# Performance work log

Hardware: AMD Instinct MI355X
Metric: run time of the kernel (lower is better)

## Reference

```python
import jax, jax.numpy as jnp
import numpy as np

DIM = 512
HEADS = 8
DH = DIM // HEADS          # 64
SCALE = DH ** (-0.5)
B, H, W = 8, 64, 64        # N = 4096, H and W multiples of 8 -> exact adaptive pool
N = H * W
POOL = 8                   # AdaptiveAvgPool2d((8,8)) -> 64 pooled tokens


def setup_inputs() -> dict:
    key = jax.random.key(0)
    ks = jax.random.split(key, 6)
    return {
        "x": jax.random.normal(ks[0], (B, N, DIM), dtype=jnp.float32),
        "proj_w": jax.random.normal(ks[1], (DIM, DIM), dtype=jnp.float32) * (DIM ** -0.5),
        "step_rep": jax.random.normal(ks[2], (HEADS, 1, 1), dtype=jnp.float32),
        "step_x": jax.random.normal(ks[3], (HEADS, 1, 1), dtype=jnp.float32),
        "to_out_w": jax.random.normal(ks[4], (DIM, DIM), dtype=jnp.float32) * (DIM ** -0.5),
        "to_out_b": jax.random.normal(ks[5], (DIM,), dtype=jnp.float32),
    }


def reference(x, proj_w, step_rep, step_x, to_out_w, to_out_b):
    b, n, c = x.shape
    # proj (Linear, no bias): w = x @ proj_w.T
    w = jnp.einsum('bnc,dc->bnd', x, proj_w)                       # [B,N,C]
    # AdaptiveAvgPool2d to (8,8): exact block mean since H,W % 8 == 0
    bh, bw = H // POOL, W // POOL
    rep = w.reshape(b, POOL, bh, POOL, bw, c).mean(axis=(2, 4))    # [B,8,8,C]
    rep = rep.reshape(b, POOL * POOL, c)                           # [B,64,C]
    # split heads: [B,h,tokens,dh]
    wh = w.reshape(b, n, HEADS, DH).transpose(0, 2, 1, 3)          # [B,h,N,dh]
    reph = rep.reshape(b, POOL * POOL, HEADS, DH).transpose(0, 2, 1, 3)  # [B,h,64,dh]
    # cross-attention: pooled queries vs full tokens (attn is reused later)
    dots = jnp.einsum('bhqd,bhkd->bhqk', reph, wh) * SCALE         # [B,h,64,N]
    attn = jax.nn.softmax(dots, axis=-1)
    rep_delta = jnp.einsum('bhqk,bhkd->bhqd', attn, wh)            # [B,h,64,dh]
    reph = reph + step_rep * rep_delta
    # self-attention among pooled reps
    dots2 = jnp.einsum('bhqd,bhkd->bhqk', reph, reph) * SCALE      # [B,h,64,64]
    attn2 = jax.nn.softmax(dots2, axis=-1)
    x_delta = jnp.einsum('bhqk,bhkd->bhqd', attn2, reph)           # [B,h,64,dh]
    # upsample back to tokens by reusing attn transposed
    x_delta = jnp.einsum('bhqn,bhqd->bhnd', attn, x_delta)         # [B,h,N,dh]
    x_delta = step_x * x_delta
    x_delta = x_delta.transpose(0, 2, 1, 3).reshape(b, n, c)       # [B,N,C]
    out = jnp.einsum('bnc,dc->bnd', x_delta, to_out_w) + to_out_b
    return out
```

## Files before the change

### kernel.cpp

```cpp
#include <hip/hip_runtime.h>
#include <hip/hip_bf16.h>
#include <stdint.h>

typedef __attribute__((ext_vector_type(8))) short short8v;
typedef __attribute__((ext_vector_type(4))) float floatx4;
typedef __attribute__((ext_vector_type(4))) unsigned uintx4;

#define DEV __device__ __forceinline__

DEV ushort f2bf(float f) {
  union { float f; unsigned u; } v; v.f = f;
  unsigned r = v.u + 0x7fffu + ((v.u >> 16) & 1u);
  return (ushort)(r >> 16);
}
DEV float bf2f(ushort b) {
  union { unsigned u; float f; } v; v.u = ((unsigned)b) << 16;
  return v.f;
}
DEV unsigned cvtpk(float lo, float hi) {
  unsigned r;
  asm("v_cvt_pk_bf16_f32 %0, %1, %2" : "=v"(r) : "v"(lo), "v"(hi));
  return r;
}
DEV int swz(int row, int colByte) {
  return row * 128 + (colByte ^ ((row & 7) << 4));
}
DEV int swz256(int row, int colByte) {
  return row * 256 + (colByte ^ ((row & 7) << 4));
}
DEV floatx4 mfma16(short8v a, short8v b, floatx4 c) {
  return __builtin_amdgcn_mfma_f32_16x16x32_bf16(a, b, c, 0, 0, 0);
}

#define GLD_LDS16(g, l)                                                   \
  __builtin_amdgcn_global_load_lds(                                       \
      (const __attribute__((address_space(1))) void*)(g),                 \
      (__attribute__((address_space(3))) void*)(l), 16, 0, 0)

#define WAIT_LGKM0 asm volatile("s_waitcnt lgkmcnt(0)" ::: "memory")
DEV void sbar() {
  __builtin_amdgcn_sched_barrier(0);
  __builtin_amdgcn_s_barrier();
  __builtin_amdgcn_sched_barrier(0);
}

constexpr int Bc = 8, HEADS = 8, NTOK = 4096, CDIM = 512, DH = 64;
constexpr float SCALE = 0.125f;
constexpr int NCH = 8, CHK = 512;

__global__ __launch_bounds__(512, 2) void k_gemm1(const float* __restrict__ A,
                                                  const float* __restrict__ Bw,
                                                  ushort* __restrict__ Cout) {
  __shared__ ushort sA[2][256 * 64];
  __shared__ ushort sB[2][256 * 64];
  const int t = threadIdx.x;
  const int w = t >> 6, l = t & 63;
  const int lg = l >> 4, li = l & 15;
  const int bid = blockIdx.x;
  const int f = (bid & 7) * 32 + (bid >> 3);
  const int m0 = (f >> 1) * 256, n0 = (f & 1) * 256;
  const int wr = (w >> 2) * 128, wc = (w & 3) * 64;

  float4 fa[8];
  float4 fb[8];

  auto loadA = [&](int kt) {
#pragma unroll
    for (int i = 0; i < 4; ++i) {
      int s = i * 512 + t, row = s >> 3, pch = s & 7;
      const float* g = A + (size_t)(m0 + row) * CDIM + kt * 64 + pch * 8;
      fa[2 * i] = *(const float4*)g;
      fa[2 * i + 1] = *(const float4*)(g + 4);
    }
  };
  auto loadB = [&](int kt) {
#pragma unroll
    for (int i = 0; i < 4; ++i) {
      int s = i * 512 + t, row = s >> 3, pch = s & 7;
      const float* g = Bw + (size_t)(n0 + row) * CDIM + kt * 64 + pch * 8;
      fb[2 * i] = *(const float4*)g;
      fb[2 * i + 1] = *(const float4*)(g + 4);
    }
  };
  auto writeAB = [&](int buf) {
#pragma unroll
    for (int i = 0; i < 4; ++i) {
      int s = i * 512 + t, row = s >> 3, pch = s & 7;
      int off = row * 128 + ((pch ^ (row & 7)) << 4);
      uintx4 pk;
      pk.x = cvtpk(fa[2 * i].x, fa[2 * i].y);
      pk.y = cvtpk(fa[2 * i].z, fa[2 * i].w);
      pk.z = cvtpk(fa[2 * i + 1].x, fa[2 * i + 1].y);
      pk.w = cvtpk(fa[2 * i + 1].z, fa[2 * i + 1].w);
      *(uintx4*)((char*)sA[buf] + off) = pk;
      uintx4 qk;
      qk.x = cvtpk(fb[2 * i].x, fb[2 * i].y);
      qk.y = cvtpk(fb[2 * i].z, fb[2 * i].w);
      qk.z = cvtpk(fb[2 * i + 1].x, fb[2 * i + 1].y);
      qk.w = cvtpk(fb[2 * i + 1].z, fb[2 * i + 1].w);
      *(uintx4*)((char*)sB[buf] + off) = qk;
    }
  };

  floatx4 acc[8][4] = {};

  loadA(0); loadB(0);
  writeAB(0);
  loadA(1); loadB(1);
  WAIT_LGKM0;
  sbar();

#pragma unroll
  for (int kt = 0; kt < 8; ++kt) {
    const int cur = kt & 1;
    if (kt < 7) writeAB(cur ^ 1);
    if (kt < 6) { loadA(kt + 2); loadB(kt + 2); }
#pragma unroll
    for (int kk = 0; kk < 2; ++kk) {
      int colb = (kk * 32 + lg * 8) * 2;
      short8v bf[4];
#pragma unroll
      for (int n = 0; n < 4; ++n)
        bf[n] = *(const short8v*)((const char*)sB[cur] + swz(wc + n * 16 + li, colb));
#pragma unroll
      for (int mh = 0; mh < 2; ++mh) {
        short8v af[4];
#pragma unroll
        for (int m = 0; m < 4; ++m)
          af[m] = *(const short8v*)((const char*)sA[cur] + swz(wr + mh * 64 + m * 16 + li, colb));
#pragma unroll
        for (int m = 0; m < 4; ++m)
#pragma unroll
          for (int n = 0; n < 4; ++n)
            acc[mh * 4 + m][n] = mfma16(af[m], bf[n], acc[mh * 4 + m][n]);
      }
    }
    if (kt < 7) { WAIT_LGKM0; sbar(); }
  }

#pragma unroll
  for (int m = 0; m < 8; ++m)
#pragma unroll
    for (int n = 0; n < 4; ++n) {
      int col = n0 + wc + n * 16 + li;
#pragma unroll
      for (int r = 0; r < 4; ++r) {
        int row = m0 + wr + m * 16 + lg * 4 + r;
        Cout[(size_t)row * CDIM + col] = f2bf(acc[m][n][r]);
      }
    }
}

__global__ __launch_bounds__(512, 2) void k_gemm3(const ushort* __restrict__ attnT,
                                                  const ushort* __restrict__ M2T,
                                                  float* __restrict__ out,
                                                  const float* __restrict__ bias) {
  __shared__ ushort sA[2][256 * 64];
  __shared__ ushort sB[2][256 * 64];
  const int t = threadIdx.x;
  const int w = t >> 6, l = t & 63;
  const int lg = l >> 4, li = l & 15;
  const int bid = blockIdx.x;
  const int b = bid & 7;
  const int idx = bid >> 3;
  const int m0 = (idx >> 1) * 256, n0 = (idx & 1) * 256;
  const int wr = (w >> 2) * 128, wc = (w & 3) * 64;
  const ushort* Bb = M2T + (size_t)b * 262144;

  short8v fA[4], fB[4];
  auto loadAB = [&](int kt) {
#pragma unroll
    for (int i = 0; i < 4; ++i) {
      int s = i * 512 + t, row = s >> 3, pch = s & 7;
      fA[i] = *(const short8v*)(attnT + (((size_t)(b * 8 + kt)) * NTOK + m0 + row) * 64 + pch * 8);
      fB[i] = *(const short8v*)(Bb + (size_t)(n0 + row) * CDIM + kt * 64 + pch * 8);
    }
  };
  auto writeAB = [&](int buf) {
#pragma unroll
    for (int i = 0; i < 4; ++i) {
      int s = i * 512 + t, row = s >> 3, pch = s & 7;
      int off = row * 128 + ((pch ^ (row & 7)) << 4);
      *(short8v*)((char*)sA[buf] + off) = fA[i];
      *(short8v*)((char*)sB[buf] + off) = fB[i];
    }
  };

  floatx4 acc[8][4] = {};

  loadAB(0);
  writeAB(0);
  loadAB(1);
  WAIT_LGKM0;
  sbar();

#pragma unroll
  for (int kt = 0; kt < 8; ++kt) {
    const int cur = kt & 1;
    if (kt < 7) writeAB(cur ^ 1);
    if (kt < 6) loadAB(kt + 2);
#pragma unroll
    for (int kk = 0; kk < 2; ++kk) {
      int colb = (kk * 32 + lg * 8) * 2;
      short8v bf[4];
#pragma unroll
      for (int n = 0; n < 4; ++n)
        bf[n] = *(const short8v*)((const char*)sB[cur] + swz(wc + n * 16 + li, colb));
#pragma unroll
      for (int mh = 0; mh < 2; ++mh) {
        short8v af[4];
#pragma unroll
        for (int m = 0; m < 4; ++m)
          af[m] = *(const short8v*)((const char*)sA[cur] + swz(wr + mh * 64 + m * 16 + li, colb));
#pragma unroll
        for (int m = 0; m < 4; ++m)
#pragma unroll
          for (int n = 0; n < 4; ++n)
            acc[mh * 4 + m][n] = mfma16(af[m], bf[n], acc[mh * 4 + m][n]);
      }
    }
    if (kt < 7) { WAIT_LGKM0; sbar(); }
  }

#pragma unroll
  for (int m = 0; m < 8; ++m)
#pragma unroll
    for (int n = 0; n < 4; ++n) {
      int col = n0 + wc + n * 16 + li;
      float bv = bias[col];
#pragma unroll
      for (int r = 0; r < 4; ++r) {
        int row = m0 + wr + m * 16 + lg * 4 + r;
        out[((size_t)b * NTOK + row) * CDIM + col] = acc[m][n][r] + bv;
      }
    }
}

__global__ __launch_bounds__(256) void k_pool(const ushort* __restrict__ wm,
                                              float* __restrict__ rep,
                                              ushort* __restrict__ qbf) {
  const int blk = blockIdx.x;
  const int b = blk >> 6, qi = blk & 63;
  const int ph = qi >> 3, pw = qi & 7;
  const int c0 = threadIdx.x * 2;
  float a0 = 0.f, a1 = 0.f;
  for (int u = 0; u < 64; ++u) {
    int n = (ph * 8 + (u >> 3)) * 64 + pw * 8 + (u & 7);
    unsigned v = *(const unsigned*)(wm + ((size_t)b * NTOK + n) * CDIM + c0);
    a0 += bf2f((ushort)(v & 0xffff));
    a1 += bf2f((ushort)(v >> 16));
  }
  a0 *= 0.015625f; a1 *= 0.015625f;
  float* dst = rep + ((size_t)b * 64 + qi) * CDIM + c0;
  dst[0] = a0;
  dst[1] = a1;
  int h = c0 >> 6, d0 = c0 & 63;
  unsigned pack = (unsigned)f2bf(a0) | ((unsigned)f2bf(a1) << 16);
  *(unsigned*)((char*)qbf + ((size_t)(b * 8 + h)) * 8192 + swz(qi, d0 * 2)) = pack;
}

__global__ __launch_bounds__(256) void k_qkexp(const ushort* __restrict__ wmat,
                                               const ushort* __restrict__ qbf,
                                               ushort* __restrict__ attnT,
                                               float* __restrict__ pvP,
                                               float* __restrict__ rsumP) {
  __shared__ char smem[57344] __attribute__((aligned(128)));
  ushort* sQ  = (ushort*)smem;
  ushort* sK  = (ushort*)(smem + 8192);
  ushort* sVT = (ushort*)(smem + 24576);
  ushort* sP  = (ushort*)(smem + 40960);

  const int bh = blockIdx.y, ch = blockIdx.x;
  const int b = bh >> 3, h = bh & 7;
  const int t = threadIdx.x, w = t >> 6, l = t & 63;
  const int lg = l >> 4, li = l & 15;

  {
    const char* qsrc = (const char*)(qbf + (size_t)bh * 4096);
#pragma unroll
    for (int i = 0; i < 2; ++i) {
      int flat = i * 256 + t;
      GLD_LDS16(qsrc + flat * 16, (char*)sQ + flat * 16);
    }
  }

  float rs[4] = {};
  floatx4 pv[4] = {};
  short8v qa[2];
  bool qaLoaded = false;

  for (int sc = 0; sc < 4; ++sc) {
    const ushort* wbase = wmat + ((size_t)b * NTOK + ch * CHK + sc * 128) * CDIM + h * DH;
    __syncthreads();
#pragma unroll
    for (int i = 0; i < 4; ++i) {
      int flat = i * 256 + t;
      int row = flat >> 3, pch = flat & 7;
      int sch = pch ^ (row & 7);
      GLD_LDS16(wbase + (size_t)row * CDIM + sch * 8, (char*)sK + flat * 16);
    }
    {
      int u = t & 63;
      int dh2 = (t >> 6) * 16;
      const ushort* g0 = wbase + (size_t)(2 * u) * CDIM + dh2;
      const ushort* g1 = g0 + CDIM;
      short8v a0 = *(const short8v*)g0;
      short8v a1 = *(const short8v*)(g0 + 8);
      short8v b0 = *(const short8v*)g1;
      short8v b1 = *(const short8v*)(g1 + 8);
#pragma unroll
      for (int j = 0; j < 8; ++j) {
        unsigned w0 = ((unsigned)(ushort)a0[j]) | (((unsigned)(ushort)b0[j]) << 16);
        *(unsigned*)((char*)sVT + swz256(dh2 + j, 4 * u)) = w0;
        unsigned w1 = ((unsigned)(ushort)a1[j]) | (((unsigned)(ushort)b1[j]) << 16);
        *(unsigned*)((char*)sVT + swz256(dh2 + 8 + j, 4 * u)) = w1;
      }
    }
    __syncthreads();

    if (!qaLoaded) {
      qaLoaded = true;
#pragma unroll
      for (int kk = 0; kk < 2; ++kk)
        qa[kk] = *(const short8v*)((const char*)sQ + swz(w * 16 + li, (kk * 32 + lg * 8) * 2));
    }

    floatx4 s[8] = {};
#pragma unroll
    for (int kk = 0; kk < 2; ++kk) {
      int cb = (kk * 32 + lg * 8) * 2;
#pragma unroll
      for (int kf = 0; kf < 8; ++kf) {
        short8v kb = *(const short8v*)((const char*)sK + swz(kf * 16 + li, cb));
        s[kf] = mfma16(qa[kk], kb, s[kf]);
      }
    }

#pragma unroll
    for (int kf = 0; kf < 8; ++kf) {
      ushort pb[4];
#pragma unroll
      for (int r = 0; r < 4; ++r) {
        float p = __expf(s[kf][r] * SCALE);
        rs[r] += p;
        pb[r] = f2bf(p);
        int q = w * 16 + lg * 4 + r;
        *(ushort*)((char*)sP + swz256(q, (kf * 16 + li) * 2)) = pb[r];
      }
      int key = ch * CHK + sc * 128 + kf * 16 + li;
      ushort4 pk; pk.x = pb[0]; pk.y = pb[1]; pk.z = pb[2]; pk.w = pb[3];
      *(ushort4*)(attnT + ((size_t)bh * NTOK + key) * 64 + w * 16 + lg * 4) = pk;
    }

#pragma unroll
    for (int kk4 = 0; kk4 < 4; ++kk4) {
      int cb = kk4 * 64 + lg * 16;
      short8v pa = *(const short8v*)((const char*)sP + swz256(w * 16 + li, cb));
#pragma unroll
      for (int nf = 0; nf < 4; ++nf) {
        short8v vb = *(const short8v*)((const char*)sVT + swz256(nf * 16 + li, cb));
        pv[nf] = mfma16(pa, vb, pv[nf]);
      }
    }
  }

#pragma unroll
  for (int r = 0; r < 4; ++r) {
    float v = rs[r];
    for (int mask = 1; mask < 16; mask <<= 1) v += __shfl_xor(v, mask);
    if (li == 0) rsumP[((size_t)bh * NCH + ch) * 64 + w * 16 + lg * 4 + r] = v;
  }
  float* pvdst = pvP + ((size_t)bh * NCH + ch) * 4096;
#pragma unroll
  for (int nf = 0; nf < 4; ++nf)
#pragma unroll
    for (int r = 0; r < 4; ++r)
      pvdst[(w * 16 + lg * 4 + r) * 64 + nf * 16 + li] = pv[nf][r];
}

__global__ __launch_bounds__(256) void k_midm2(const float* __restrict__ rep,
                                               const float* __restrict__ pvP,
                                               const float* __restrict__ rsumP,
                                               const float* __restrict__ step_rep,
                                               const float* __restrict__ step_x,
                                               const float* __restrict__ tow,
                                               ushort* __restrict__ m2t) {
  __shared__ float sSum[64];
  __shared__ float sRd[4096];
  __shared__ float sR[64 * 65];
  __shared__ float sT[64 * 65];
  __shared__ ushort sXd[4096];
  const int bh = blockIdx.x;
  const int b = bh >> 3, h = bh & 7;
  const int t = threadIdx.x, w = t >> 6, l = t & 63;
  const int lg = l >> 4, li = l & 15;

  if (t < 64) {
    float v = 0.f;
#pragma unroll
    for (int ch = 0; ch < NCH; ++ch) v += rsumP[((size_t)bh * NCH + ch) * 64 + t];
    sSum[t] = v;
  }
  {
    const float* p = pvP + (size_t)bh * NCH * 4096;
#pragma unroll
    for (int j = 0; j < 16; ++j) {
      int idx = t + 256 * j;
      float sm = 0.f;
#pragma unroll
      for (int ch = 0; ch < NCH; ++ch) sm += p[ch * 4096 + idx];
      sRd[idx] = sm;
    }
  }
  __syncthreads();
  {
    int q = t >> 2, d0 = (t & 3) * 16;
    float srep = step_rep[h];
    float inv = 1.f / sSum[q];
    const float* rp = rep + ((size_t)b * 64 + q) * CDIM + h * DH + d0;
#pragma unroll
    for (int j = 0; j < 16; ++j) sR[q * 65 + d0 + j] = rp[j] + srep * (sRd[q * 64 + d0 + j] * inv);
  }
  __syncthreads();
  {
    int q = t >> 2, jb = (t & 3) * 16;
    float a[16];
#pragma unroll
    for (int j = 0; j < 16; ++j) {
      float accd = 0.f;
      for (int d = 0; d < 64; ++d) accd += sR[q * 65 + d] * sR[(jb + j) * 65 + d];
      a[j] = accd * SCALE;
    }
    float mx = a[0];
#pragma unroll
    for (int j = 1; j < 16; ++j) mx = fmaxf(mx, a[j]);
    mx = fmaxf(mx, __shfl_xor(mx, 1));
    mx = fmaxf(mx, __shfl_xor(mx, 2));
    float sm = 0.f;
#pragma unroll
    for (int j = 0; j < 16; ++j) { a[j] = __expf(a[j] - mx); sm += a[j]; }
    sm += __shfl_xor(sm, 1);
    sm += __shfl_xor(sm, 2);
    float inv = 1.f / sm;
#pragma unroll
    for (int j = 0; j < 16; ++j) sT[q * 65 + jb + j] = a[j] * inv;
  }
  __syncthreads();
  {
    int q = t >> 2, db = (t & 3) * 16;
    float accd[16] = {};
    for (int j = 0; j < 64; ++j) {
      float w2 = sT[q * 65 + j];
#pragma unroll
      for (int d = 0; d < 16; ++d) accd[d] += w2 * sR[j * 65 + db + d];
    }
    float sc = step_x[h] / sSum[q];
    ushort o[16] __attribute__((aligned(16)));
#pragma unroll
    for (int d = 0; d < 16; ++d) o[d] = f2bf(accd[d] * sc);
    *(short8v*)((char*)sXd + swz(q, db * 2)) = *(short8v*)&o[0];
    *(short8v*)((char*)sXd + swz(q, db * 2 + 16)) = *(short8v*)&o[8];
  }
  __syncthreads();
  floatx4 acc[8][4] = {};
#pragma unroll
  for (int kk = 0; kk < 2; ++kk) {
    int dd0 = kk * 32 + lg * 8;
    short8v bf[4];
#pragma unroll
    for (int nf = 0; nf < 4; ++nf)
      bf[nf] = *(const short8v*)((const char*)sXd + swz(nf * 16 + li, dd0 * 2));
#pragma unroll
    for (int m = 0; m < 8; ++m) {
      int d = w * 128 + m * 16 + li;
      const float* g = tow + (size_t)d * CDIM + h * DH + dd0;
      float4 lo = *(const float4*)g;
      float4 hi = *(const float4*)(g + 4);
      uintx4 u;
      u.x = cvtpk(lo.x, lo.y); u.y = cvtpk(lo.z, lo.w);
      u.z = cvtpk(hi.x, hi.y); u.w = cvtpk(hi.z, hi.w);
      short8v af = *(short8v*)&u;
#pragma unroll
      for (int nf = 0; nf < 4; ++nf) acc[m][nf] = mfma16(af, bf[nf], acc[m][nf]);
    }
  }
#pragma unroll
  for (int m = 0; m < 8; ++m)
#pragma unroll
    for (int nf = 0; nf < 4; ++nf)
#pragma unroll
      for (int r = 0; r < 4; ++r) {
        int d = w * 128 + m * 16 + lg * 4 + r;
        int hq = h * 64 + nf * 16 + li;
        m2t[((size_t)b * CDIM + d) * CDIM + hq] = f2bf(acc[m][nf][r]);
      }
}

extern "C" void kernel_launch(void* const* d_in, const int* in_sizes, int n_in,
                              void* d_out, int out_size, void* d_ws, size_t ws_size,
                              hipStream_t stream) {
  const float* x = (const float*)d_in[0];
  const float* proj_w = (const float*)d_in[1];
  const float* step_rep = (const float*)d_in[2];
  const float* step_x = (const float*)d_in[3];
  const float* to_out_w = (const float*)d_in[4];
  const float* to_out_b = (const float*)d_in[5];
  float* out = (float*)d_out;
  char* ws = (char*)d_ws;
  char* ob = (char*)d_out;

  ushort* bufA = (ushort*)(ws);
  ushort* bufB = (ushort*)(ws + 33554432);
  float*  rep  = (float*)(ws + 68157440);
  float*  pvP   = (float*)(ob);
  ushort* qbf   = (ushort*)(ob + 34603008);
  float*  rsumP = (float*)(ob + 35127296);
  ushort* m2t   = bufB;

  k_gemm1<<<256, 512, 0, stream>>>(x, proj_w, bufB);

  k_pool<<<Bc * 64, 256, 0, stream>>>(bufB, rep, qbf);

  k_qkexp<<<dim3(NCH, Bc * HEADS), 256, 0, stream>>>(bufB, qbf, bufA, pvP, rsumP);

  k_midm2<<<Bc * HEADS, 256, 0, stream>>>(rep, pvP, rsumP, step_rep, step_x, to_out_w, m2t);

  k_gemm3<<<256, 512, 0, stream>>>(bufA, m2t, out, to_out_b);
}
```

Before: 107.7 us.

## Recompute attention probabilities inside final GEMM instead of storing attnT

The cross-attention kernel no longer writes the unnormalized bf16 probability matrix to global memory. The final GEMM now reloads the projected tokens and pooled queries per head, recomputes QK^T and exp into shared memory, and feeds that tile into the output GEMM. This trades a large global write and read of the attention matrix for extra MFMA and exp work plus per-head barriers. The final kernel also drops its register double-buffering and runs at occupancy 1 with more shared memory.

```diff
diff --git a/kernel.cpp b/kernel.cpp
--- a/kernel.cpp
+++ b/kernel.cpp
@@ -151,12 +151,17 @@
     }
 }
 
-__global__ __launch_bounds__(512, 2) void k_gemm3(const ushort* __restrict__ attnT,
-                                                  const ushort* __restrict__ M2T,
-                                                  float* __restrict__ out,
-                                                  const float* __restrict__ bias) {
-  __shared__ ushort sA[2][256 * 64];
-  __shared__ ushort sB[2][256 * 64];
+__global__ __launch_bounds__(512, 1) void k_gemm3r(const ushort* __restrict__ wmat,
+                                                   const ushort* __restrict__ qbf,
+                                                   const ushort* __restrict__ M2T,
+                                                   float* __restrict__ out,
+                                                   const float* __restrict__ bias) {
+  __shared__ char smem[106496] __attribute__((aligned(128)));
+  char* wA   = smem;
+  char* sB   = smem + 32768;
+  char* sP   = smem + 65536;
+  char* sRep = smem + 98304;
+
   const int t = threadIdx.x;
   const int w = t >> 6, l = t & 63;
   const int lg = l >> 4, li = l & 15;
@@ -165,53 +170,70 @@
   const int idx = bid >> 3;
   const int m0 = (idx >> 1) * 256, n0 = (idx & 1) * 256;
   const int wr = (w >> 2) * 128, wc = (w & 3) * 64;
-  const ushort* Bb = M2T + (size_t)b * 262144;
-
-  short8v fA[4], fB[4];
-  auto loadAB = [&](int kt) {
+
+  floatx4 acc[8][4] = {};
+
+  for (int h = 0; h < 8; ++h) {
+    __syncthreads();
 #pragma unroll
     for (int i = 0; i < 4; ++i) {
-      int s = i * 512 + t, row = s >> 3, pch = s & 7;
-      fA[i] = *(const short8v*)(attnT + (((size_t)(b * 8 + kt)) * NTOK + m0 + row) * 64 + pch * 8);
-      fB[i] = *(const short8v*)(Bb + (size_t)(n0 + row) * CDIM + kt * 64 + pch * 8);
-    }
-  };
-  auto writeAB = [&](int buf) {
+      int flat = i * 512 + t, row = flat >> 3, pch = flat & 7;
+      int sch = pch ^ (row & 7);
+      GLD_LDS16(wmat + ((size_t)(b * NTOK + m0 + row)) * CDIM + h * 64 + sch * 8,
+                wA + flat * 16);
+    }
 #pragma unroll
     for (int i = 0; i < 4; ++i) {
-      int s = i * 512 + t, row = s >> 3, pch = s & 7;
-      int off = row * 128 + ((pch ^ (row & 7)) << 4);
-      *(short8v*)((char*)sA[buf] + off) = fA[i];
-      *(short8v*)((char*)sB[buf] + off) = fB[i];
-    }
-  };
-
-  floatx4 acc[8][4] = {};
-
-  loadAB(0);
-  writeAB(0);
-  loadAB(1);
-  WAIT_LGKM0;
-  sbar();
-
-#pragma unroll
-  for (int kt = 0; kt < 8; ++kt) {
-    const int cur = kt & 1;
-    if (kt < 7) writeAB(cur ^ 1);
-    if (kt < 6) loadAB(kt + 2);
+      int flat = i * 512 + t, row = flat >> 3, pch = flat & 7;
+      int sch = pch ^ (row & 7);
+      GLD_LDS16(M2T + (size_t)b * 262144 + (size_t)(n0 + row) * CDIM + h * 64 + sch * 8,
+                sB + flat * 16);
+    }
+    GLD_LDS16((const char*)(qbf + (size_t)(b * 8 + h) * 4096) + t * 16, sRep + t * 16);
+    __syncthreads();
+
+    floatx4 s[2][4] = {};
+#pragma unroll
+    for (int kk2 = 0; kk2 < 2; ++kk2) {
+      int colb = (kk2 * 32 + lg * 8) * 2;
+      short8v rb[4];
+#pragma unroll
+      for (int qf = 0; qf < 4; ++qf)
+        rb[qf] = *(const short8v*)(sRep + swz(qf * 16 + li, colb));
+#pragma unroll
+      for (int mf = 0; mf < 2; ++mf) {
+        short8v ra = *(const short8v*)(wA + swz(w * 32 + mf * 16 + li, colb));
+#pragma unroll
+        for (int qf = 0; qf < 4; ++qf)
+          s[mf][qf] = mfma16(ra, rb[qf], s[mf][qf]);
+      }
+    }
+#pragma unroll
+    for (int mf = 0; mf < 2; ++mf)
+#pragma unroll
+      for (int qf = 0; qf < 4; ++qf)
+#pragma unroll
+        for (int r = 0; r < 4; ++r) {
+          float p = __expf(s[mf][qf][r] * SCALE);
+          int tok = w * 32 + mf * 16 + lg * 4 + r;
+          int q = qf * 16 + li;
+          *(ushort*)(sP + swz(tok, 2 * q)) = f2bf(p);
+        }
+    __syncthreads();
+
 #pragma unroll
     for (int kk = 0; kk < 2; ++kk) {
       int colb = (kk * 32 + lg * 8) * 2;
       short8v bf[4];
 #pragma unroll
       for (int n = 0; n < 4; ++n)
-        bf[n] = *(const short8v*)((const char*)sB[cur] + swz(wc + n * 16 + li, colb));
+        bf[n] = *(const short8v*)(sB + swz(wc + n * 16 + li, colb));
 #pragma unroll
       for (int mh = 0; mh < 2; ++mh) {
         short8v af[4];
 #pragma unroll
         for (int m = 0; m < 4; ++m)
-          af[m] = *(const short8v*)((const char*)sA[cur] + swz(wr + mh * 64 + m * 16 + li, colb));
+          af[m] = *(const short8v*)(sP + swz(wr + mh * 64 + m * 16 + li, colb));
 #pragma unroll
         for (int m = 0; m < 4; ++m)
 #pragma unroll
@@ -219,7 +241,6 @@
             acc[mh * 4 + m][n] = mfma16(af[m], bf[n], acc[mh * 4 + m][n]);
       }
     }
-    if (kt < 7) { WAIT_LGKM0; sbar(); }
   }
 
 #pragma unroll
@@ -261,7 +282,6 @@
 
 __global__ __launch_bounds__(256) void k_qkexp(const ushort* __restrict__ wmat,
                                                const ushort* __restrict__ qbf,
-                                               ushort* __restrict__ attnT,
                                                float* __restrict__ pvP,
                                                float* __restrict__ rsumP) {
   __shared__ char smem[57344] __attribute__((aligned(128)));
@@ -338,18 +358,13 @@
 
 #pragma unroll
     for (int kf = 0; kf < 8; ++kf) {
-      ushort pb[4];
 #pragma unroll
       for (int r = 0; r < 4; ++r) {
         float p = __expf(s[kf][r] * SCALE);
         rs[r] += p;
-        pb[r] = f2bf(p);
         int q = w * 16 + lg * 4 + r;
-        *(ushort*)((char*)sP + swz256(q, (kf * 16 + li) * 2)) = pb[r];
-      }
-      int key = ch * CHK + sc * 128 + kf * 16 + li;
-      ushort4 pk; pk.x = pb[0]; pk.y = pb[1]; pk.z = pb[2]; pk.w = pb[3];
-      *(ushort4*)(attnT + ((size_t)bh * NTOK + key) * 64 + w * 16 + lg * 4) = pk;
+        *(ushort*)((char*)sP + swz256(q, (kf * 16 + li) * 2)) = f2bf(p);
+      }
     }
 
 #pragma unroll
@@ -509,21 +524,20 @@
   char* ws = (char*)d_ws;
   char* ob = (char*)d_out;
 
-  ushort* bufA = (ushort*)(ws);
-  ushort* bufB = (ushort*)(ws + 33554432);
-  float*  rep  = (float*)(ws + 68157440);
+  ushort* bufW = (ushort*)(ws);
+  ushort* m2t  = (ushort*)(ws + 33554432);
+  ushort* qbf  = (ushort*)(ws + 37748736);
+  float*  rep  = (float*)(ws + 38273024);
   float*  pvP   = (float*)(ob);
-  ushort* qbf   = (ushort*)(ob + 34603008);
-  float*  rsumP = (float*)(ob + 35127296);
-  ushort* m2t   = bufB;
-
-  k_gemm1<<<256, 512, 0, stream>>>(x, proj_w, bufB);
-
-  k_pool<<<Bc * 64, 256, 0, stream>>>(bufB, rep, qbf);
-
-  k_qkexp<<<dim3(NCH, Bc * HEADS), 256, 0, stream>>>(bufB, qbf, bufA, pvP, rsumP);
+  float*  rsumP = (float*)(ob + 8388608);
+
+  k_gemm1<<<256, 512, 0, stream>>>(x, proj_w, bufW);
+
+  k_pool<<<Bc * 64, 256, 0, stream>>>(bufW, rep, qbf);
+
+  k_qkexp<<<dim3(NCH, Bc * HEADS), 256, 0, stream>>>(bufW, qbf, pvP, rsumP);
 
   k_midm2<<<Bc * HEADS, 256, 0, stream>>>(rep, pvP, rsumP, step_rep, step_x, to_out_w, m2t);
 
-  k_gemm3<<<256, 512, 0, stream>>>(bufA, m2t, out, to_out_b);
-}
+  k_gemm3r<<<256, 512, 0, stream>>>(bufW, qbf, m2t, out, to_out_b);
+}
```

After: 115.9 us. 7.7% more time.
